# Kernel tuning notes

Hardware: AMD Instinct MI355X
Metric: run time of the kernel (lower is better)

The kernel has to match this reference:

```python
import jax, jax.numpy as jnp
import numpy as np

N_NODES = 20000
N_EDGES = 320000
NEG_SLOPE = 0.2


def gat_conv(x, src, dst, W, a_src, a_dst, b, concat):
    # x: [N, Fin]; W: [Fin, H*C]; a_src/a_dst: [H, C]; b: [H*C] or [C]
    N = x.shape[0]
    H, C = a_src.shape
    h = (x @ W).reshape(N, H, C)                      # [N, H, C]
    al_s = jnp.einsum('nhc,hc->nh', h, a_src)         # [N, H]
    al_d = jnp.einsum('nhc,hc->nh', h, a_dst)         # [N, H]
    e = jax.nn.leaky_relu(al_s[src] + al_d[dst], NEG_SLOPE)  # [E, H]
    # segment softmax over incoming edges of each dst node
    m = jax.ops.segment_max(e, dst, num_segments=N)   # [N, H]
    ex = jnp.exp(e - m[dst])
    denom = jax.ops.segment_sum(ex, dst, num_segments=N)
    alpha = ex / denom[dst]                           # [E, H]
    msg = alpha[:, :, None] * h[src]                  # [E, H, C]
    out = jax.ops.segment_sum(msg, dst, num_segments=N)  # [N, H, C]
    if concat:
        return out.reshape(N, H * C) + b
    return out.mean(axis=1) + b


def setup_inputs() -> dict:
    key = jax.random.key(0)
    ks = jax.random.split(key, 16)
    def g(k, shape, scale=0.05):
        return jax.random.normal(k, shape, dtype=jnp.float32) * scale
    x = jax.random.normal(ks[0], (N_NODES, 768), dtype=jnp.float32)
    edge_index = jax.random.randint(ks[1], (2, N_EDGES), 0, N_NODES, dtype=jnp.int32)
    return {
        'x': x, 'edge_index': edge_index,
        'W1': g(ks[2], (768, 1024)), 'a1_src': g(ks[3], (4, 256)), 'a1_dst': g(ks[4], (4, 256)), 'b1': g(ks[5], (1024,)),
        'W2': g(ks[6], (1024, 512)), 'a2_src': g(ks[7], (4, 128)), 'a2_dst': g(ks[8], (4, 128)), 'b2': g(ks[9], (512,)),
        'W3': g(ks[10], (512, 64)), 'a3_src': g(ks[11], (1, 64)), 'a3_dst': g(ks[12], (1, 64)), 'b3': g(ks[13], (64,)),
    }


def reference(x, edge_index, W1, a1_src, a1_dst, b1, W2, a2_src, a2_dst, b2, W3, a3_src, a3_dst, b3):
    N = x.shape[0]
    loops = jnp.arange(N, dtype=edge_index.dtype)
    src = jnp.concatenate([edge_index[0], loops])  # PyG GATConv adds self-loops
    dst = jnp.concatenate([edge_index[1], loops])
    h = gat_conv(x, src, dst, W1, a1_src, a1_dst, b1, concat=True)
    h = jax.nn.relu(h)
    h = gat_conv(h, src, dst, W2, a2_src, a2_dst, b2, concat=True)
    h = jax.nn.relu(h)
    h = gat_conv(h, src, dst, W3, a3_src, a3_dst, b3, concat=False)
    return jnp.tanh(h)
```

## Files before the change

kernel.cpp:

```cpp
#include <hip/hip_runtime.h>
#include <hip/hip_bf16.h>

#define NN 20000
#define NE 320000
#define ET 340000
#define NEG_SLOPE 0.2f

typedef __attribute__((ext_vector_type(8))) _Float16 f16x8;
typedef __attribute__((ext_vector_type(4))) _Float16 f16x4;
typedef __attribute__((ext_vector_type(4))) float f32x4;

typedef __attribute__((address_space(3))) unsigned int lds_u32_t;
typedef __attribute__((address_space(1))) unsigned int glb_u32_t;

__device__ __forceinline__ void gload_lds16(const void* g, void* l) {
  __builtin_amdgcn_global_load_lds((const glb_u32_t*)g, (lds_u32_t*)l, 16, 0, 0);
}

__global__ __launch_bounds__(256) void k_init(
    const float* __restrict__ x, _Float16* __restrict__ xb,
    int* __restrict__ cnt, float* __restrict__ zb, int nz,
    const float* __restrict__ W1, _Float16* __restrict__ Wt1,
    const float* __restrict__ W2, _Float16* __restrict__ Wt2,
    const float* __restrict__ W3, _Float16* __restrict__ Wt3) {
  __shared__ float tile[32][33];
  if (blockIdx.x < 1312) {
    int b = blockIdx.x;
    const float* W; _Float16* Wt; int K, N, bk, bn;
    if (b < 768)       { W = W1; Wt = Wt1; K = 768;  N = 1024; bn = (b % 32) * 32; bk = (b / 32) * 32; }
    else if (b < 1280) { b -= 768;  W = W2; Wt = Wt2; K = 1024; N = 512; bn = (b % 16) * 32; bk = (b / 16) * 32; }
    else               { b -= 1280; W = W3; Wt = Wt3; K = 512;  N = 64;  bn = (b % 2) * 32;  bk = (b / 2) * 32; }
    int tx = threadIdx.x & 31, ty = threadIdx.x >> 5;
#pragma unroll
    for (int r = ty; r < 32; r += 8)
      tile[r][tx] = W[(size_t)(bk + r) * N + bn + tx];
    __syncthreads();
#pragma unroll
    for (int r = ty; r < 32; r += 8)
      Wt[(size_t)(bn + r) * K + bk + tx] = (_Float16)tile[tx][r];
    return;
  }
  const int stride = (gridDim.x - 1312) * blockDim.x;
  const int i0 = (blockIdx.x - 1312) * blockDim.x + threadIdx.x;
  for (int i = i0; i < NN; i += stride) cnt[i] = 0;
  for (int i = i0; i < nz; i += stride) zb[i] = 0.f;
  const int n4 = NN * 768 / 4;
  for (int i = i0; i < n4; i += stride) {
    f32x4 v = *(const f32x4*)&x[i * 4];
    f16x4 h = { (_Float16)v.x, (_Float16)v.y, (_Float16)v.z, (_Float16)v.w };
    *(f16x4*)&xb[i * 4] = h;
  }
}

__global__ void k_count(const int* __restrict__ ei, int* __restrict__ cnt) {
  int e = blockIdx.x * blockDim.x + threadIdx.x;
  if (e >= ET) return;
  int d = (e < NE) ? ei[NE + e] : (e - NE);
  atomicAdd(&cnt[d], 1);
}

__global__ __launch_bounds__(1024) void k_scan(const int* __restrict__ cnt,
                                               int* __restrict__ rptr,
                                               int* __restrict__ cursor) {
  const int CH = 20;
  int t = threadIdx.x, lane = t & 63, wid = t >> 6;
  int base = t * CH;
  int v[CH];
  int sum = 0;
#pragma unroll
  for (int j = 0; j < CH; ++j) {
    int idx = base + j;
    v[j] = (idx < NN) ? cnt[idx] : 0;
    sum += v[j];
  }
  int ws = sum;
#pragma unroll
  for (int off = 1; off < 64; off <<= 1) {
    int u = __shfl_up(ws, off);
    if (lane >= off) ws += u;
  }
  __shared__ int wsum[16];
  __shared__ int wpre[16];
  if (lane == 63) wsum[wid] = ws;
  __syncthreads();
  if (t == 0) {
    int acc = 0;
#pragma unroll
    for (int w = 0; w < 16; ++w) { wpre[w] = acc; acc += wsum[w]; }
  }
  __syncthreads();
  int run = wpre[wid] + ws - sum;
  if (t == 0) rptr[0] = 0;
#pragma unroll
  for (int j = 0; j < CH; ++j) {
    int idx = base + j;
    if (idx < NN) {
      cursor[idx] = run;
      run += v[j];
      rptr[idx + 1] = run;
    }
  }
}

__global__ void k_fill(const int* __restrict__ ei, int* __restrict__ cursor,
                       int* __restrict__ csrc) {
  int e = blockIdx.x * blockDim.x + threadIdx.x;
  if (e >= ET) return;
  int s, d;
  if (e < NE) { s = ei[e]; d = ei[NE + e]; } else { s = d = e - NE; }
  int p = atomicAdd(&cursor[d], 1);
  csrc[p] = s;
}

__global__ __launch_bounds__(256) void k_gemm(const _Float16* __restrict__ A,
                                              const _Float16* __restrict__ B,
                                              _Float16* __restrict__ C,
                                              const float* __restrict__ a_src,
                                              const float* __restrict__ a_dst,
                                              float* __restrict__ als,
                                              float* __restrict__ ald,
                                              int M, int N, int K, int gx,
                                              int H, int Ch) {
  const int nb = gridDim.x;
  const int q = nb >> 3, r = nb & 7;
  const int xcd = blockIdx.x & 7, kk = blockIdx.x >> 3;
  const int l = (xcd < r) ? (xcd * (q + 1) + kk) : (r * (q + 1) + (xcd - r) * q + kk);
  const int bx = l % gx, by = l / gx;

  __shared__ __align__(16) _Float16 Al[128 * 32];
  __shared__ __align__(16) _Float16 Bl[128 * 32];
  const int tid = threadIdx.x;
  const int wave = tid >> 6, lane = tid & 63;
  const int wm = wave >> 1, wn = wave & 1;
  const int m0 = by * 128, n0 = bx * 128;
  const int fr = lane & 15, fk = (lane >> 4) * 8;
  f32x4 acc[4][4] = {};

  for (int k0 = 0; k0 < K; k0 += 32) {
#pragma unroll
    for (int c = 0; c < 2; ++c) {
      int s = (wave * 2 + c) * 64 + lane;
      int row = s >> 2, col = (s & 3) * 8;
      int ra = m0 + row; if (ra > M - 1) ra = M - 1;
      int rb = n0 + row; if (rb > N - 1) rb = N - 1;
      gload_lds16(A + (size_t)ra * K + k0 + col, &Al[(size_t)(wave * 2 + c) * 512]);
      gload_lds16(B + (size_t)rb * K + k0 + col, &Bl[(size_t)(wave * 2 + c) * 512]);
    }
    __syncthreads();
    f16x8 af[4], bf[4];
#pragma unroll
    for (int i = 0; i < 4; ++i) {
      af[i] = *(const f16x8*)&Al[(wm * 64 + i * 16 + fr) * 32 + fk];
      bf[i] = *(const f16x8*)&Bl[(wn * 64 + i * 16 + fr) * 32 + fk];
    }
#pragma unroll
    for (int mi = 0; mi < 4; ++mi)
#pragma unroll
      for (int ni = 0; ni < 4; ++ni)
        acc[mi][ni] = __builtin_amdgcn_mfma_f32_16x16x32_f16(af[mi], bf[ni], acc[mi][ni], 0, 0, 0);
    __syncthreads();
  }

  const int r0 = (lane >> 4) * 4, cn = lane & 15;

#pragma unroll
  for (int mi = 0; mi < 4; ++mi)
#pragma unroll
    for (int ni = 0; ni < 4; ++ni) {
      int gm = m0 + wm * 64 + mi * 16 + r0;
      int gn = n0 + wn * 64 + ni * 16 + cn;
      if (gn < N) {
#pragma unroll
        for (int rr = 0; rr < 4; ++rr)
          if (gm + rr < M) C[(size_t)(gm + rr) * N + gn] = (_Float16)acc[mi][ni][rr];
      }
    }

  const int colbase = n0 + wn * 64;
  if (colbase < N) {
    const int hd = colbase / Ch;
    const int cin = colbase % Ch;
    float asv[4], adv[4];
#pragma unroll
    for (int ni = 0; ni < 4; ++ni) {
      int cc = colbase + ni * 16 + cn;
      bool ok = cc < N;
      int ci = hd * Ch + cin + ni * 16 + cn;
      asv[ni] = ok ? a_src[ci] : 0.f;
      adv[ni] = ok ? a_dst[ci] : 0.f;
    }
#pragma unroll
    for (int mi = 0; mi < 4; ++mi) {
#pragma unroll
      for (int rr = 0; rr < 4; ++rr) {
        float sv = 0.f, dv = 0.f;
#pragma unroll
        for (int ni = 0; ni < 4; ++ni) {
          sv += acc[mi][ni][rr] * asv[ni];
          dv += acc[mi][ni][rr] * adv[ni];
        }
#pragma unroll
        for (int off = 1; off < 16; off <<= 1) {
          sv += __shfl_xor(sv, off);
          dv += __shfl_xor(dv, off);
        }
        if ((lane & 15) == 0) {
          int gm = m0 + wm * 64 + mi * 16 + r0 + rr;
          if (gm < M) {
            atomicAdd(&als[gm * H + hd], sv);
            atomicAdd(&ald[gm * H + hd], dv);
          }
        }
      }
    }
  }
}

template <int H, int C, int MODE>
__global__ __launch_bounds__(256) void k_aggw(
    const _Float16* __restrict__ h, const float* __restrict__ als,
    const float* __restrict__ ald, const int* __restrict__ rptr,
    const int* __restrict__ csrc, const float* __restrict__ bias,
    _Float16* __restrict__ oh, float* __restrict__ of, int nbase) {
  constexpr int HC = H * C;
  constexpr int CPL = HC / 64;
  constexpr int NV = CPL / 8;
  const int wave = threadIdx.x >> 6, lane = threadIdx.x & 63;
  const int n = nbase + blockIdx.x * 4 + wave;
  const int c0 = lane * CPL;
  const int hd = c0 / C;
  const float aldn = ald[n * H + hd];
  const int e0 = rptr[n], e1 = rptr[n + 1];
  float acc[CPL];
#pragma unroll
  for (int j = 0; j < CPL; ++j) acc[j] = 0.f;
  float den = 0.f;

  float lA = 0.f, lB = 0.f;
  f16x8 hA[NV], hB[NV];

#define LD_ROW(I, L, HV)                                                     \
  do {                                                                       \
    int _i = (I);                                                            \
    if (_i < e1) {                                                           \
      int _s = csrc[_i];                                                     \
      (L) = als[_s * H + hd];                                                \
      const _Float16* _hp = h + (size_t)_s * HC + c0;                        \
      _Pragma("unroll")                                                      \
      for (int _v = 0; _v < NV; ++_v) (HV)[_v] = *(const f16x8*)(_hp + _v * 8); \
    }                                                                        \
  } while (0)

  LD_ROW(e0, lA, hA);
  LD_ROW(e0 + 1, lB, hB);

  for (int i = e0; i < e1; i += 2) {
    {
      float v = lA + aldn;
      f16x8 t[NV];
#pragma unroll
      for (int vv = 0; vv < NV; ++vv) t[vv] = hA[vv];
      LD_ROW(i + 2, lA, hA);
      v = v > 0.f ? v : NEG_SLOPE * v;
      float xv = __expf(v);
      den += xv;
#pragma unroll
      for (int vv = 0; vv < NV; ++vv)
#pragma unroll
        for (int j = 0; j < 8; ++j) acc[vv * 8 + j] += xv * (float)t[vv][j];
    }
    if (i + 1 < e1) {
      float v = lB + aldn;
      f16x8 t[NV];
#pragma unroll
      for (int vv = 0; vv < NV; ++vv) t[vv] = hB[vv];
      LD_ROW(i + 3, lB, hB);
      v = v > 0.f ? v : NEG_SLOPE * v;
      float xv = __expf(v);
      den += xv;
#pragma unroll
      for (int vv = 0; vv < NV; ++vv)
#pragma unroll
        for (int j = 0; j < 8; ++j) acc[vv * 8 + j] += xv * (float)t[vv][j];
    }
  }
#undef LD_ROW

  float invd = 1.f / den;
#pragma unroll
  for (int v = 0; v < NV; ++v) {
    f16x8 o;
#pragma unroll
    for (int j = 0; j < 8; ++j) {
      float r = acc[v * 8 + j] * invd + bias[c0 + v * 8 + j];
      o[j] = (_Float16)(r > 0.f ? r : 0.f);
    }
    __builtin_nontemporal_store(o, (f16x8*)&oh[(size_t)n * HC + c0 + v * 8]);
  }
}

__global__ __launch_bounds__(256) void k_agg_last(
    const _Float16* __restrict__ h, const float* __restrict__ als,
    const float* __restrict__ ald, const int* __restrict__ rptr,
    const int* __restrict__ csrc, const float* __restrict__ bias,
    float* __restrict__ of) {
  int wave = threadIdx.x >> 6, t = threadIdx.x & 63;
  int n = blockIdx.x * 4 + wave;
  float acc = 0.f, den = 0.f;
  float aldn = ald[n];
  int e0 = rptr[n], e1 = rptr[n + 1];
  for (int i = e0; i < e1; ++i) {
    int s = csrc[i];
    float v = als[s] + aldn;
    v = v > 0.f ? v : NEG_SLOPE * v;
    float xv = __expf(v);
    den += xv;
    acc += xv * (float)h[(size_t)s * 64 + t];
  }
  of[(size_t)n * 64 + t] = tanhf(acc / den + bias[t]);
}

static inline size_t alup(size_t x) { return (x + 255) & ~(size_t)255; }

struct Scratch {
  _Float16* xb; _Float16* wtb1; _Float16* wtb2; _Float16* wtb3; _Float16* h;
  float* zb;
  int* cnt; int* rptr; int* cursor; int* csrc;
};

static void run_layer(hipStream_t stream, const Scratch& S, const _Float16* xin,
                      const _Float16* wtb, float* als, float* ald,
                      int K, int N, int H, int C,
                      const float* as_, const float* ad_, const float* bias,
                      int mode, _Float16* oh, float* of) {
  int gx = (N + 127) / 128, gy = (NN + 127) / 128;
  k_gemm<<<gx * gy, 256, 0, stream>>>(xin, wtb, S.h, as_, ad_, als, ald,
                                      NN, N, K, gx, H, C);
  if (mode == 0) {
    if (C == 256) {
      k_aggw<4, 256, 0><<<NN / 8, 256, 0, stream>>>(S.h, als, ald, S.rptr, S.csrc, bias, oh, of, 0);
      k_aggw<4, 256, 0><<<NN / 8, 256, 0, stream>>>(S.h, als, ald, S.rptr, S.csrc, bias, oh, of, NN / 2);
    } else if (C == 128) {
      k_aggw<4, 128, 0><<<NN / 4, 256, 0, stream>>>(S.h, als, ald, S.rptr, S.csrc, bias, oh, of, 0);
    }
  } else {
    k_agg_last<<<NN / 4, 256, 0, stream>>>(S.h, als, ald, S.rptr, S.csrc, bias, of);
  }
}

extern "C" void kernel_launch(void* const* d_in, const int* in_sizes, int n_in,
                              void* d_out, int out_size, void* d_ws, size_t ws_size,
                              hipStream_t stream) {
  const float* x   = (const float*)d_in[0];
  const int*   ei  = (const int*)d_in[1];
  const float* W1  = (const float*)d_in[2];
  const float* a1s = (const float*)d_in[3];
  const float* a1d = (const float*)d_in[4];
  const float* b1  = (const float*)d_in[5];
  const float* W2  = (const float*)d_in[6];
  const float* a2s = (const float*)d_in[7];
  const float* a2d = (const float*)d_in[8];
  const float* b2  = (const float*)d_in[9];
  const float* W3  = (const float*)d_in[10];
  const float* a3s = (const float*)d_in[11];
  const float* a3d = (const float*)d_in[12];
  const float* b3  = (const float*)d_in[13];
  float* out = (float*)d_out;

  char* p = (char*)d_ws;
  Scratch S;
  S.xb   = (_Float16*)p; p += alup((size_t)NN * 1024 * 2);
  S.wtb1 = (_Float16*)p; p += alup((size_t)1024 * 768 * 2);
  S.wtb2 = (_Float16*)p; p += alup((size_t)512 * 1024 * 2);
  S.wtb3 = (_Float16*)p; p += alup((size_t)64 * 512 * 2);
  S.h    = (_Float16*)p; p += alup((size_t)NN * 1024 * 2);
  S.zb   = (float*)p;    p += alup((size_t)NN * 18 * 4);
  S.cnt  = (int*)p;      p += alup((size_t)NN * 4);
  S.rptr = (int*)p;      p += alup((size_t)(NN + 1) * 4);
  S.cursor=(int*)p;      p += alup((size_t)NN * 4);
  S.csrc = (int*)p;      p += alup((size_t)ET * 4);

  float* als1 = S.zb;
  float* ald1 = als1 + NN * 4;
  float* als2 = ald1 + NN * 4;
  float* ald2 = als2 + NN * 4;
  float* als3 = ald2 + NN * 4;
  float* ald3 = als3 + NN;

  k_init<<<1312 + 1024, 256, 0, stream>>>(x, S.xb, S.cnt, S.zb, NN * 18,
                                          W1, S.wtb1, W2, S.wtb2, W3, S.wtb3);
  k_count<<<(ET + 255) / 256, 256, 0, stream>>>(ei, S.cnt);
  k_scan<<<1, 1024, 0, stream>>>(S.cnt, S.rptr, S.cursor);
  k_fill<<<(ET + 255) / 256, 256, 0, stream>>>(ei, S.cursor, S.csrc);

  run_layer(stream, S, S.xb, S.wtb1, als1, ald1, 768, 1024, 4, 256, a1s, a1d, b1, 0, S.xb, nullptr);
  run_layer(stream, S, S.xb, S.wtb2, als2, ald2, 1024, 512, 4, 128, a2s, a2d, b2, 0, S.xb, nullptr);
  run_layer(stream, S, S.xb, S.wtb3, als3, ald3, 512, 64, 1, 64, a3s, a3d, b3, 1, nullptr, out);
}
```

Baseline: 440.9 us.

## Double-buffer GEMM LDS tiles with XOR swizzle and merge split aggregation launch

The GEMM main loop now uses two LDS buffers so the next K-slice is fetched with direct global-to-LDS loads while MFMAs run on the current slice, leaving one barrier per iteration instead of two. The LDS column layout is XOR-swizzled by row to reduce bank conflicts on the fragment reads. The layer-1 aggregation, previously split into two half launches, becomes a single launch over all nodes. Doubling LDS use per block may lower occupancy, and the swizzle has to match exactly between the stage writes and the fragment reads.

```diff
diff --git a/kernel.cpp b/kernel.cpp
--- a/kernel.cpp
+++ b/kernel.cpp
@@ -127,39 +127,58 @@
   const int l = (xcd < r) ? (xcd * (q + 1) + kk) : (r * (q + 1) + (xcd - r) * q + kk);
   const int bx = l % gx, by = l / gx;
 
-  __shared__ __align__(16) _Float16 Al[128 * 32];
-  __shared__ __align__(16) _Float16 Bl[128 * 32];
+  __shared__ __align__(16) _Float16 Al[2][128 * 32];
+  __shared__ __align__(16) _Float16 Bl[2][128 * 32];
   const int tid = threadIdx.x;
   const int wave = tid >> 6, lane = tid & 63;
   const int wm = wave >> 1, wn = wave & 1;
   const int m0 = by * 128, n0 = bx * 128;
-  const int fr = lane & 15, fk = (lane >> 4) * 8;
+  const int fr = lane & 15;
+  const int fx = ((lane >> 4) ^ ((fr >> 1) & 3)) * 8;
   f32x4 acc[4][4] = {};
 
-  for (int k0 = 0; k0 < K; k0 += 32) {
-#pragma unroll
-    for (int c = 0; c < 2; ++c) {
-      int s = (wave * 2 + c) * 64 + lane;
-      int row = s >> 2, col = (s & 3) * 8;
-      int ra = m0 + row; if (ra > M - 1) ra = M - 1;
-      int rb = n0 + row; if (rb > N - 1) rb = N - 1;
-      gload_lds16(A + (size_t)ra * K + k0 + col, &Al[(size_t)(wave * 2 + c) * 512]);
-      gload_lds16(B + (size_t)rb * K + k0 + col, &Bl[(size_t)(wave * 2 + c) * 512]);
-    }
+#define STAGE(BUF, K0)                                                        \
+  do {                                                                        \
+    _Pragma("unroll")                                                         \
+    for (int c = 0; c < 2; ++c) {                                             \
+      int s = (wave * 2 + c) * 64 + lane;                                     \
+      int row = s >> 2;                                                       \
+      int col = ((s & 3) ^ ((s >> 3) & 3)) * 8;                               \
+      int ra = m0 + row; if (ra > M - 1) ra = M - 1;                          \
+      int rb = n0 + row; if (rb > N - 1) rb = N - 1;                          \
+      gload_lds16(A + (size_t)ra * K + (K0) + col, &Al[BUF][(wave * 2 + c) * 512]); \
+      gload_lds16(B + (size_t)rb * K + (K0) + col, &Bl[BUF][(wave * 2 + c) * 512]); \
+    }                                                                         \
+  } while (0)
+
+#define COMPUTE(BUF)                                                          \
+  do {                                                                        \
+    f16x8 af[4], bf[4];                                                       \
+    _Pragma("unroll")                                                         \
+    for (int i = 0; i < 4; ++i) {                                             \
+      af[i] = *(const f16x8*)&Al[BUF][(wm * 64 + i * 16 + fr) * 32 + fx];     \
+      bf[i] = *(const f16x8*)&Bl[BUF][(wn * 64 + i * 16 + fr) * 32 + fx];     \
+    }                                                                         \
+    _Pragma("unroll")                                                         \
+    for (int mi = 0; mi < 4; ++mi)                                            \
+      _Pragma("unroll")                                                       \
+      for (int ni = 0; ni < 4; ++ni)                                          \
+        acc[mi][ni] = __builtin_amdgcn_mfma_f32_16x16x32_f16(af[mi], bf[ni], acc[mi][ni], 0, 0, 0); \
+  } while (0)
+
+  STAGE(0, 0);
+  __syncthreads();
+  int cur = 0;
+  for (int k0 = 32; k0 < K; k0 += 32) {
+    STAGE(cur ^ 1, k0);
+    COMPUTE(cur);
     __syncthreads();
-    f16x8 af[4], bf[4];
-#pragma unroll
-    for (int i = 0; i < 4; ++i) {
-      af[i] = *(const f16x8*)&Al[(wm * 64 + i * 16 + fr) * 32 + fk];
-      bf[i] = *(const f16x8*)&Bl[(wn * 64 + i * 16 + fr) * 32 + fk];
-    }
-#pragma unroll
-    for (int mi = 0; mi < 4; ++mi)
-#pragma unroll
-      for (int ni = 0; ni < 4; ++ni)
-        acc[mi][ni] = __builtin_amdgcn_mfma_f32_16x16x32_f16(af[mi], bf[ni], acc[mi][ni], 0, 0, 0);
-    __syncthreads();
-  }
+    cur ^= 1;
+  }
+  COMPUTE(cur);
+
+#undef STAGE
+#undef COMPUTE
 
   const int r0 = (lane >> 4) * 4, cn = lane & 15;
 
@@ -221,12 +240,12 @@
     const _Float16* __restrict__ h, const float* __restrict__ als,
     const float* __restrict__ ald, const int* __restrict__ rptr,
     const int* __restrict__ csrc, const float* __restrict__ bias,
-    _Float16* __restrict__ oh, float* __restrict__ of, int nbase) {
+    _Float16* __restrict__ oh, float* __restrict__ of) {
   constexpr int HC = H * C;
   constexpr int CPL = HC / 64;
   constexpr int NV = CPL / 8;
   const int wave = threadIdx.x >> 6, lane = threadIdx.x & 63;
-  const int n = nbase + blockIdx.x * 4 + wave;
+  const int n = blockIdx.x * 4 + wave;
   const int c0 = lane * CPL;
   const int hd = c0 / C;
   const float aldn = ald[n * H + hd];
@@ -337,12 +356,8 @@
   k_gemm<<<gx * gy, 256, 0, stream>>>(xin, wtb, S.h, as_, ad_, als, ald,
                                       NN, N, K, gx, H, C);
   if (mode == 0) {
-    if (C == 256) {
-      k_aggw<4, 256, 0><<<NN / 8, 256, 0, stream>>>(S.h, als, ald, S.rptr, S.csrc, bias, oh, of, 0);
-      k_aggw<4, 256, 0><<<NN / 8, 256, 0, stream>>>(S.h, als, ald, S.rptr, S.csrc, bias, oh, of, NN / 2);
-    } else if (C == 128) {
-      k_aggw<4, 128, 0><<<NN / 4, 256, 0, stream>>>(S.h, als, ald, S.rptr, S.csrc, bias, oh, of, 0);
-    }
+    if (C == 256)      k_aggw<4, 256, 0><<<NN / 4, 256, 0, stream>>>(S.h, als, ald, S.rptr, S.csrc, bias, oh, of);
+    else if (C == 128) k_aggw<4, 128, 0><<<NN / 4, 256, 0, stream>>>(S.h, als, ald, S.rptr, S.csrc, bias, oh, of);
   } else {
     k_agg_last<<<NN / 4, 256, 0, stream>>>(S.h, als, ald, S.rptr, S.csrc, bias, of);
   }
```

New measurement: 432.0 us. 2.0% less time.
